# Kernel tuning notes

Measured on AMD Instinct MI355X. Metric: run time of the kernel, lower is better.

Reference implementation:

```python
import jax, jax.numpy as jnp
import numpy as np

NLON = 720  # output longitude points for irfft
B, C = 4, 8
LMAX, MMAX, NLAT = 360, 361, 361


def setup_inputs() -> dict:
    key = jax.random.key(0)
    kx, kd = jax.random.split(key)
    # x: real view of complex coeffs, shape [B, C, 2(vec comp), lmax, mmax, 2(re/im)]
    x = jax.random.normal(kx, (B, C, 2, LMAX, MMAX, 2), dtype=jnp.float32)
    # dpct: precomputed dLegendre buffer, shape [2, mmax, lmax, nlat]
    dpct = jax.random.normal(kd, (2, MMAX, LMAX, NLAT), dtype=jnp.float32) * 0.1
    return {"x": x, "dpct": dpct}


def reference(x, dpct):
    # split vector components and real/imag parts
    x0r = x[..., 0, :, :, 0]  # [..., lmax, mmax]
    x0i = x[..., 0, :, :, 1]
    x1r = x[..., 1, :, :, 0]
    x1i = x[..., 1, :, :, 1]
    d0 = dpct[0].astype(x.dtype)  # [mmax, lmax, nlat]
    d1 = dpct[1].astype(x.dtype)

    def ein(a, d):
        return jnp.einsum('...lm,mlk->...km', a, d)

    srl = ein(x0r, d0) - ein(x1i, d1)   # [..., nlat, mmax]
    sim = ein(x0i, d0) + ein(x1r, d1)
    trl = -ein(x0i, d1) - ein(x1r, d0)
    tim = ein(x0r, d1) - ein(x1i, d0)

    s = jax.lax.complex(srl, sim)
    t = jax.lax.complex(trl, tim)
    xs = jnp.stack((s, t), axis=-3)     # [..., 2, nlat, mmax] complex
    # inverse real FFT over longitude, 'forward' norm (no scaling on inverse)
    out = jnp.fft.irfft(xs, n=NLON, axis=-1, norm='forward')  # [..., 2, nlat, nlon]
    return out
```

## Files before the change

kernel.cpp:

```cpp
#include <hip/hip_runtime.h>
#include <hip/hip_bf16.h>
#include <math.h>

#define LMAX 360
#define MMAX 361
#define NLAT 361
#define NLON 720
#define BC   32
#define MT   (BC*2*NLAT)
#define NLATP 364
#define MTP  (BC*2*NLATP)
#define QT   722
#define KP   736
#define NP   768
#define BM   128
#define BN   128
#define BK   32

typedef __attribute__((ext_vector_type(8))) short short8;
typedef __attribute__((ext_vector_type(4))) short short4v;
typedef __attribute__((ext_vector_type(4))) float f32x4;

static __device__ __forceinline__ short f2bf(float v) {
    __hip_bfloat16 h = __float2bfloat16(v);
    return *reinterpret_cast<short*>(&h);
}

__global__ __launch_bounds__(256) void sht_prep_x(
    const float* __restrict__ x, __hip_bfloat16* __restrict__ xT)
{
    const int m0 = blockIdx.x * 32;
    const int l0 = blockIdx.y * 64;
    const int bc = blockIdx.z >> 1, f = blockIdx.z & 1;
    __shared__ float2 tile[64][33];
    const float2* __restrict__ x2 = (const float2*)x;
    const int t = threadIdx.x;
    const int rm = t & 31, rl = t >> 5;

    const int mm = min(m0 + rm, MMAX - 1);
    #pragma unroll
    for (int r = 0; r < 8; ++r) {
        int l = min(l0 + rl + r * 8, LMAX - 1);
        tile[rl + r * 8][rm] = x2[((size_t)(bc * 2 + f) * LMAX + l) * MMAX + mm];
    }
    __syncthreads();

    const int tm = t >> 3, lg = t & 7;
    const int m = m0 + tm;
    if (m >= MMAX) return;
    const int lw = l0 + lg * 8;
    if (lw >= LMAX) return;

    short8 re, im;
    #pragma unroll
    for (int e = 0; e < 8; ++e) {
        float2 v = tile[lg * 8 + e][tm];
        re[e] = f2bf(v.x);
        im[e] = f2bf(v.y);
    }
    size_t mb = (size_t)m * (128 * LMAX);
    *(short8*)((short*)xT + mb + (size_t)((f * 2 + 0) * 32 + bc) * LMAX + lw) = re;
    *(short8*)((short*)xT + mb + (size_t)((f * 2 + 1) * 32 + bc) * LMAX + lw) = im;
}

__global__ __launch_bounds__(256, 3) void sht_gemm1(
    const float* __restrict__ dpct, const __hip_bfloat16* __restrict__ xT,
    __hip_bfloat16* __restrict__ interQ)
{
    const int m  = blockIdx.x;
    const int K0 = blockIdx.y * 96;

    __shared__ __align__(16) char AlsB[96 * 128];
    __shared__ __align__(16) char BlsB[128 * 128];

    const int t    = threadIdx.x;
    const int lane = t & 63;
    const int wave = t >> 6;
    const int wm = (wave >> 1) * 48;
    const int wn = (wave & 1) * 64;
    const int fr = lane & 15;
    const int lq = lane >> 4;

    int kdv[3], lov[3], kcl[3];
    #pragma unroll
    for (int it = 0; it < 3; ++it) {
        int task = it * 256 + t;
        kdv[it] = task % 96;
        lov[it] = task / 96;
        kcl[it] = min(K0 + kdv[it], 360);
    }
    const int cB    = t >> 1;
    const int plane = cB >> 5, bcq = cB & 31;
    const int g0B   = (t & 1) * 4;

    const int            srcT[8] = {0, 1, 2, 3, 3, 2, 1, 0};
    const unsigned short sgnT[8] = {0, 0, 0x8000, 0x8000, 0x8000, 0, 0x8000, 0};

    f32x4 acc[3][4];
    const f32x4 zero = {0.f, 0.f, 0.f, 0.f};
    #pragma unroll
    for (int i = 0; i < 3; ++i)
        #pragma unroll
        for (int j = 0; j < 4; ++j) acc[i][j] = zero;

    float a0_[3][8], a1_[3][8];
    bool  v0_[3],    v1_[3];
    short8 bpf[4];
    bool   bvB[4];
    short  bsgn = 0;

#define STEP_P(s)  ((s) >= 6 ? 1 : 0)
#define STEP_L(s)  (((s) % 6) * 64)

#define LOAD_A(AP, LV, ss) {                                                   \
    const int p_ = STEP_P(ss); const int l0_ = STEP_L(ss);                     \
    const size_t rowb_ = ((size_t)p_ * MMAX + m) * LMAX;                       \
    _Pragma("unroll")                                                          \
    for (int it = 0; it < 3; ++it) {                                           \
        int lb_ = l0_ + lov[it] * 8;                                           \
        LV[it] = (lb_ < LMAX);                                                 \
        int lcl_ = LV[it] ? lb_ : 0;                                           \
        const float* sp_ = dpct + (rowb_ + lcl_) * (size_t)NLAT + kcl[it];     \
        _Pragma("unroll")                                                      \
        for (int e = 0; e < 8; ++e)                                            \
            AP[it][e] = sp_[(size_t)e * NLAT];                                 \
    } }

#define LOAD_B(ss) {                                                           \
    const int p_ = STEP_P(ss); const int l0_ = STEP_L(ss);                     \
    int src_ = srcT[p_ * 4 + plane];                                           \
    bsgn = (short)sgnT[p_ * 4 + plane];                                        \
    const short* bb_ = (const short*)xT + (size_t)m * (128 * LMAX) +           \
                       (size_t)(src_ * 32 + bcq) * LMAX;                       \
    _Pragma("unroll")                                                          \
    for (int i = 0; i < 4; ++i) {                                              \
        int lg2_ = l0_ + (g0B + i) * 8;                                        \
        bvB[i] = (lg2_ < LMAX);                                                \
        int lcl_ = bvB[i] ? lg2_ : 0;                                          \
        bpf[i] = *(const short8*)(bb_ + lcl_);                                 \
    } }

#define WRITE_A(AP, LV) {                                                      \
    _Pragma("unroll")                                                          \
    for (int it = 0; it < 3; ++it) {                                           \
        short8 w_;                                                             \
        _Pragma("unroll")                                                      \
        for (int e = 0; e < 8; ++e)                                            \
            w_[e] = LV[it] ? f2bf(AP[it][e]) : (short)0;                       \
        int kd_ = kdv[it], lo_ = lov[it];                                      \
        *(short8*)(AlsB + kd_ * 128 + ((lo_ ^ (kd_ & 7)) << 4)) = w_;          \
    } }

#define WRITE_B() {                                                            \
    _Pragma("unroll")                                                          \
    for (int i = 0; i < 4; ++i) {                                              \
        short8 v_ = bpf[i];                                                    \
        _Pragma("unroll")                                                      \
        for (int e = 0; e < 8; ++e) {                                          \
            short xe_ = (short)(v_[e] ^ bsgn);                                 \
            v_[e] = bvB[i] ? xe_ : (short)0;                                   \
        }                                                                      \
        int g_ = g0B + i;                                                      \
        *(short8*)(BlsB + cB * 128 + ((g_ ^ (cB & 7)) << 4)) = v_;             \
    } }

    auto compute = [&]() {
        #pragma unroll
        for (int kk = 0; kk < 2; ++kk) {
            short8 af[3], bg[4];
            const int g = kk * 4 + lq;
            #pragma unroll
            for (int mi = 0; mi < 3; ++mi) {
                int k = wm + mi * 16 + fr;
                af[mi] = *(const short8*)(AlsB + k * 128 + ((g ^ (k & 7)) << 4));
            }
            #pragma unroll
            for (int ni = 0; ni < 4; ++ni) {
                int c = wn + ni * 16 + fr;
                bg[ni] = *(const short8*)(BlsB + c * 128 + ((g ^ (c & 7)) << 4));
            }
            #pragma unroll
            for (int mi = 0; mi < 3; ++mi)
                #pragma unroll
                for (int ni = 0; ni < 4; ++ni)
                    acc[mi][ni] = __builtin_amdgcn_mfma_f32_16x16x32_bf16(
                        af[mi], bg[ni], acc[mi][ni], 0, 0, 0);
        }
    };

    LOAD_B(0);
    LOAD_A(a0_, v0_, 0);
    LOAD_A(a1_, v1_, 1);

    #pragma unroll 1
    for (int s = 0; s < 12; s += 2) {
        __syncthreads();
        WRITE_A(a0_, v0_);
        WRITE_B();
        __syncthreads();
        if (s + 1 < 12) LOAD_B(s + 1);
        if (s + 2 < 12) LOAD_A(a0_, v0_, s + 2);
        compute();

        __syncthreads();
        WRITE_A(a1_, v1_);
        WRITE_B();
        __syncthreads();
        if (s + 2 < 12) LOAD_B(s + 2);
        if (s + 3 < 12) LOAD_A(a1_, v1_, s + 3);
        compute();
    }

#undef LOAD_A
#undef LOAD_B
#undef WRITE_A
#undef WRITE_B
#undef STEP_P
#undef STEP_L

    #pragma unroll
    for (int mi = 0; mi < 3; ++mi) {
        int kr = K0 + wm + mi * 16 + lq * 4;
        #pragma unroll
        for (int ni = 0; ni < 4; ++ni) {
            int c = wn + ni * 16 + fr;
            int pl = c >> 5, bc = c & 31;
            int ri = pl & 1, tt = pl >> 1;
            size_t qb = (size_t)(2 * m + ri) * MTP + (size_t)(bc * 2 + tt) * NLATP;
            if (kr + 3 <= 360) {
                short4v w;
                #pragma unroll
                for (int r = 0; r < 4; ++r) w[r] = f2bf(acc[mi][ni][r]);
                *(short4v*)((short*)interQ + qb + kr) = w;
            } else if (kr <= 360) {
                ((short*)interQ)[qb + kr] = f2bf(acc[mi][ni][0]);
            }
        }
    }
}

__global__ __launch_bounds__(256) void sht_transpose(
    const __hip_bfloat16* __restrict__ inQ, __hip_bfloat16* __restrict__ outT)
{
    __shared__ __hip_bfloat16 tile[64][65];
    const int R0 = blockIdx.x * 64;
    const int q0 = blockIdx.y * 64;
    const int tx = threadIdx.x & 63;
    const int ty = threadIdx.x >> 6;
    const __hip_bfloat16 zv = __float2bfloat16(0.f);

    const int R  = R0 + tx;
    const int Rm = (R / NLAT) * NLATP + (R % NLAT);

    for (int qq = ty; qq < 64; qq += 4) {
        int q = q0 + qq;
        tile[qq][tx] = (q < QT) ? inQ[(size_t)q * MTP + Rm] : zv;
    }
    __syncthreads();
    if (q0 + tx < KP) {
        for (int rr = ty; rr < 64; rr += 4) {
            outT[(size_t)(R0 + rr) * KP + q0 + tx] = tile[tx][rr];
        }
    }
}

__global__ __launch_bounds__(256) void sht_make_w(__hip_bfloat16* __restrict__ W)
{
    const int idx = blockIdx.x * 256 + threadIdx.x;
    const int j = idx / KP;
    const int q = idx % KP;
    float v = 0.f;
    if (j < NLON && q < QT) {
        int m = q >> 1;
        float coef = (m == 0 || m == 360) ? 1.f : 2.f;
        int ph = (m * j) % 720;
        float ang = (float)ph * (float)(2.0 * M_PI / 720.0);
        float s, c;
        __sincosf(ang, &s, &c);
        v = (q & 1) ? (-coef * s) : (coef * c);
    }
    W[idx] = __float2bfloat16(v);
}

__global__ __launch_bounds__(256) void sht_gemm(
    const __hip_bfloat16* __restrict__ A,
    const __hip_bfloat16* __restrict__ W,
    float* __restrict__ out)
{
    __shared__ __align__(16) __hip_bfloat16 As[BM * BK];
    __shared__ __align__(16) __hip_bfloat16 Bs[BN * BK];
    const int t  = threadIdx.x;
    const int R0 = blockIdx.x * BM;
    const int J0 = blockIdx.y * BN;

    const int rowA = t >> 2;
    const int kc   = (t & 3) * 8;
    const int gr0  = min(R0 + rowA,      MT - 1);
    const int gr1  = min(R0 + rowA + 64, MT - 1);
    const __hip_bfloat16* pa0 = A + (size_t)gr0 * KP + kc;
    const __hip_bfloat16* pa1 = A + (size_t)gr1 * KP + kc;
    const __hip_bfloat16* pb0 = W + (size_t)(J0 + rowA) * KP + kc;
    const __hip_bfloat16* pb1 = W + (size_t)(J0 + rowA + 64) * KP + kc;

    const int lane = t & 63;
    const int wave = t >> 6;
    const int wm = (wave >> 1) * 64;
    const int wn = (wave & 1) * 64;
    const int fr = lane & 15;
    const int kg = (lane >> 4) * 8;

    f32x4 acc[4][4];
    const f32x4 zero = {0.f, 0.f, 0.f, 0.f};
    #pragma unroll
    for (int i = 0; i < 4; ++i)
        #pragma unroll
        for (int j = 0; j < 4; ++j) acc[i][j] = zero;

    short8 va0 = *(const short8*)pa0;
    short8 va1 = *(const short8*)pa1;
    short8 vb0 = *(const short8*)pb0;
    short8 vb1 = *(const short8*)pb1;

    for (int kt = 0; kt < KP / BK; ++kt) {
        __syncthreads();
        *(short8*)&As[t * 8]        = va0;
        *(short8*)&As[t * 8 + 2048] = va1;
        *(short8*)&Bs[t * 8]        = vb0;
        *(short8*)&Bs[t * 8 + 2048] = vb1;
        __syncthreads();

        if (kt + 1 < KP / BK) {
            const int ko = (kt + 1) * BK;
            va0 = *(const short8*)(pa0 + ko);
            va1 = *(const short8*)(pa1 + ko);
            vb0 = *(const short8*)(pb0 + ko);
            vb1 = *(const short8*)(pb1 + ko);
        }

        short8 af[4], bg[4];
        #pragma unroll
        for (int i = 0; i < 4; ++i)
            af[i] = *(const short8*)&As[(wm + i * 16 + fr) * BK + kg];
        #pragma unroll
        for (int i = 0; i < 4; ++i)
            bg[i] = *(const short8*)&Bs[(wn + i * 16 + fr) * BK + kg];

        #pragma unroll
        for (int mi = 0; mi < 4; ++mi)
            #pragma unroll
            for (int ni = 0; ni < 4; ++ni)
                acc[mi][ni] = __builtin_amdgcn_mfma_f32_16x16x32_bf16(
                    af[mi], bg[ni], acc[mi][ni], 0, 0, 0);
    }

    const int orow = (lane >> 4) * 4;
    #pragma unroll
    for (int mi = 0; mi < 4; ++mi) {
        #pragma unroll
        for (int ni = 0; ni < 4; ++ni) {
            #pragma unroll
            for (int r = 0; r < 4; ++r) {
                int row = R0 + wm + mi * 16 + orow + r;
                int col = J0 + wn + ni * 16 + fr;
                if (row < MT && col < NLON)
                    out[(size_t)row * NLON + col] = acc[mi][ni][r];
            }
        }
    }
}

extern "C" void kernel_launch(void* const* d_in, const int* in_sizes, int n_in,
                              void* d_out, int out_size, void* d_ws, size_t ws_size,
                              hipStream_t stream)
{
    const float* x    = (const float*)d_in[0];
    const float* dpct = (const float*)d_in[1];
    float* out        = (float*)d_out;

    char* ws = (char*)d_ws;
    __hip_bfloat16* xT     = (__hip_bfloat16*)ws;
    __hip_bfloat16* interT = (__hip_bfloat16*)(ws + 34009088);
    __hip_bfloat16* interQ = (__hip_bfloat16*)(ws + 70254592);
    __hip_bfloat16* Wt     = (__hip_bfloat16*)(ws + 104857600);

    dim3 gp(12, 6, 64);
    sht_prep_x<<<gp, 256, 0, stream>>>(x, xT);

    dim3 g1(MMAX, 4);
    sht_gemm1<<<g1, 256, 0, stream>>>(dpct, xT, interQ);

    dim3 gt(MT / 64, 12);
    sht_transpose<<<gt, 256, 0, stream>>>(interQ, interT);

    sht_make_w<<<(NP * KP) / 256, 256, 0, stream>>>(Wt);

    dim3 gg((MT + BM - 1) / BM, NP / BN);
    sht_gemm<<<gg, 256, 0, stream>>>(interT, Wt, out);
}
```

Before: 322.0 us.

## Load both Legendre planes per step and reuse each x tile across them

Each pipeline step of the first GEMM now loads both dpct planes into two shared-memory A tiles and loads the x tile once. The source-plane permutation and sign flip are applied when B fragments are read during compute, instead of when B is staged. This halves the number of steps and barriers and removes the second global load of the same x tile. In exchange it uses more shared memory and registers, which may lower occupancy under the 3-blocks launch bound, and adds XOR work to the inner loop.

```diff
diff --git a/kernel.cpp b/kernel.cpp
--- a/kernel.cpp
+++ b/kernel.cpp
@@ -70,7 +70,8 @@
     const int m  = blockIdx.x;
     const int K0 = blockIdx.y * 96;
 
-    __shared__ __align__(16) char AlsB[96 * 128];
+    __shared__ __align__(16) char Als0[96 * 128];
+    __shared__ __align__(16) char Als1[96 * 128];
     __shared__ __align__(16) char BlsB[128 * 128];
 
     const int t    = threadIdx.x;
@@ -89,9 +90,8 @@
         lov[it] = task / 96;
         kcl[it] = min(K0 + kdv[it], 360);
     }
-    const int cB    = t >> 1;
-    const int plane = cB >> 5, bcq = cB & 31;
-    const int g0B   = (t & 1) * 4;
+    const int cB  = t >> 1;
+    const int g0B = (t & 1) * 4;
 
     const int            srcT[8] = {0, 1, 2, 3, 3, 2, 1, 0};
     const unsigned short sgnT[8] = {0, 0, 0x8000, 0x8000, 0x8000, 0, 0x8000, 0};
@@ -103,63 +103,56 @@
         #pragma unroll
         for (int j = 0; j < 4; ++j) acc[i][j] = zero;
 
-    float a0_[3][8], a1_[3][8];
-    bool  v0_[3],    v1_[3];
+    float  a0_[3][8], a1_[3][8];
+    bool   av_[3];
     short8 bpf[4];
     bool   bvB[4];
-    short  bsgn = 0;
-
-#define STEP_P(s)  ((s) >= 6 ? 1 : 0)
-#define STEP_L(s)  (((s) % 6) * 64)
-
-#define LOAD_A(AP, LV, ss) {                                                   \
-    const int p_ = STEP_P(ss); const int l0_ = STEP_L(ss);                     \
-    const size_t rowb_ = ((size_t)p_ * MMAX + m) * LMAX;                       \
-    _Pragma("unroll")                                                          \
-    for (int it = 0; it < 3; ++it) {                                           \
-        int lb_ = l0_ + lov[it] * 8;                                           \
-        LV[it] = (lb_ < LMAX);                                                 \
-        int lcl_ = LV[it] ? lb_ : 0;                                           \
-        const float* sp_ = dpct + (rowb_ + lcl_) * (size_t)NLAT + kcl[it];     \
-        _Pragma("unroll")                                                      \
-        for (int e = 0; e < 8; ++e)                                            \
-            AP[it][e] = sp_[(size_t)e * NLAT];                                 \
-    } }
-
-#define LOAD_B(ss) {                                                           \
-    const int p_ = STEP_P(ss); const int l0_ = STEP_L(ss);                     \
-    int src_ = srcT[p_ * 4 + plane];                                           \
-    bsgn = (short)sgnT[p_ * 4 + plane];                                        \
+
+#define LOAD_AB(ss) {                                                          \
+    const int l0_ = (ss) * 64;                                                 \
     const short* bb_ = (const short*)xT + (size_t)m * (128 * LMAX) +           \
-                       (size_t)(src_ * 32 + bcq) * LMAX;                       \
+                       (size_t)cB * LMAX;                                      \
     _Pragma("unroll")                                                          \
     for (int i = 0; i < 4; ++i) {                                              \
         int lg2_ = l0_ + (g0B + i) * 8;                                        \
         bvB[i] = (lg2_ < LMAX);                                                \
         int lcl_ = bvB[i] ? lg2_ : 0;                                          \
         bpf[i] = *(const short8*)(bb_ + lcl_);                                 \
-    } }
-
-#define WRITE_A(AP, LV) {                                                      \
+    }                                                                          \
     _Pragma("unroll")                                                          \
     for (int it = 0; it < 3; ++it) {                                           \
-        short8 w_;                                                             \
+        int lb_ = l0_ + lov[it] * 8;                                           \
+        av_[it] = (lb_ < LMAX);                                                \
+        int lcl_ = av_[it] ? lb_ : 0;                                          \
+        const float* s0_ = dpct + ((size_t)m * LMAX + lcl_) * NLAT + kcl[it];  \
+        const float* s1_ = dpct + (((size_t)MMAX + m) * LMAX + lcl_) * NLAT    \
+                           + kcl[it];                                          \
         _Pragma("unroll")                                                      \
-        for (int e = 0; e < 8; ++e)                                            \
-            w_[e] = LV[it] ? f2bf(AP[it][e]) : (short)0;                       \
+        for (int e = 0; e < 8; ++e) {                                          \
+            a0_[it][e] = s0_[(size_t)e * NLAT];                                \
+            a1_[it][e] = s1_[(size_t)e * NLAT];                                \
+        }                                                                      \
+    } }
+
+#define WRITE_AB() {                                                           \
+    _Pragma("unroll")                                                          \
+    for (int it = 0; it < 3; ++it) {                                           \
+        short8 w0_, w1_;                                                       \
+        _Pragma("unroll")                                                      \
+        for (int e = 0; e < 8; ++e) {                                          \
+            w0_[e] = av_[it] ? f2bf(a0_[it][e]) : (short)0;                    \
+            w1_[e] = av_[it] ? f2bf(a1_[it][e]) : (short)0;                    \
+        }                                                                      \
         int kd_ = kdv[it], lo_ = lov[it];                                      \
-        *(short8*)(AlsB + kd_ * 128 + ((lo_ ^ (kd_ & 7)) << 4)) = w_;          \
-    } }
-
-#define WRITE_B() {                                                            \
+        int off_ = kd_ * 128 + ((lo_ ^ (kd_ & 7)) << 4);                       \
+        *(short8*)(Als0 + off_) = w0_;                                         \
+        *(short8*)(Als1 + off_) = w1_;                                         \
+    }                                                                          \
     _Pragma("unroll")                                                          \
     for (int i = 0; i < 4; ++i) {                                              \
         short8 v_ = bpf[i];                                                    \
         _Pragma("unroll")                                                      \
-        for (int e = 0; e < 8; ++e) {                                          \
-            short xe_ = (short)(v_[e] ^ bsgn);                                 \
-            v_[e] = bvB[i] ? xe_ : (short)0;                                   \
-        }                                                                      \
+        for (int e = 0; e < 8; ++e) v_[e] = bvB[i] ? v_[e] : (short)0;         \
         int g_ = g0B + i;                                                      \
         *(short8*)(BlsB + cB * 128 + ((g_ ^ (cB & 7)) << 4)) = v_;             \
     } }
@@ -167,56 +160,48 @@
     auto compute = [&]() {
         #pragma unroll
         for (int kk = 0; kk < 2; ++kk) {
-            short8 af[3], bg[4];
             const int g = kk * 4 + lq;
+            short8 af0[3], af1[3];
             #pragma unroll
             for (int mi = 0; mi < 3; ++mi) {
                 int k = wm + mi * 16 + fr;
-                af[mi] = *(const short8*)(AlsB + k * 128 + ((g ^ (k & 7)) << 4));
+                int off = k * 128 + ((g ^ (k & 7)) << 4);
+                af0[mi] = *(const short8*)(Als0 + off);
+                af1[mi] = *(const short8*)(Als1 + off);
             }
             #pragma unroll
-            for (int ni = 0; ni < 4; ++ni) {
-                int c = wn + ni * 16 + fr;
-                bg[ni] = *(const short8*)(BlsB + c * 128 + ((g ^ (c & 7)) << 4));
+            for (int h = 0; h < 2; ++h) {
+                #pragma unroll
+                for (int ni = 0; ni < 4; ++ni) {
+                    int pl = 2 * (wave & 1) + (ni >> 1);
+                    int rB = srcT[h * 4 + pl] * 32 + (ni & 1) * 16 + fr;
+                    short8 bg = *(const short8*)(
+                        BlsB + rB * 128 + ((g ^ (rB & 7)) << 4));
+                    short sg = (short)sgnT[h * 4 + pl];
+                    #pragma unroll
+                    for (int e = 0; e < 8; ++e) bg[e] ^= sg;
+                    #pragma unroll
+                    for (int mi = 0; mi < 3; ++mi)
+                        acc[mi][ni] = __builtin_amdgcn_mfma_f32_16x16x32_bf16(
+                            h ? af1[mi] : af0[mi], bg, acc[mi][ni], 0, 0, 0);
+                }
             }
-            #pragma unroll
-            for (int mi = 0; mi < 3; ++mi)
-                #pragma unroll
-                for (int ni = 0; ni < 4; ++ni)
-                    acc[mi][ni] = __builtin_amdgcn_mfma_f32_16x16x32_bf16(
-                        af[mi], bg[ni], acc[mi][ni], 0, 0, 0);
         }
     };
 
-    LOAD_B(0);
-    LOAD_A(a0_, v0_, 0);
-    LOAD_A(a1_, v1_, 1);
+    LOAD_AB(0);
 
     #pragma unroll 1
-    for (int s = 0; s < 12; s += 2) {
+    for (int s = 0; s < 6; ++s) {
         __syncthreads();
-        WRITE_A(a0_, v0_);
-        WRITE_B();
+        WRITE_AB();
         __syncthreads();
-        if (s + 1 < 12) LOAD_B(s + 1);
-        if (s + 2 < 12) LOAD_A(a0_, v0_, s + 2);
+        if (s < 5) LOAD_AB(s + 1);
         compute();
-
-        __syncthreads();
-        WRITE_A(a1_, v1_);
-        WRITE_B();
-        __syncthreads();
-        if (s + 2 < 12) LOAD_B(s + 2);
-        if (s + 3 < 12) LOAD_A(a1_, v1_, s + 3);
-        compute();
-    }
-
-#undef LOAD_A
-#undef LOAD_B
-#undef WRITE_A
-#undef WRITE_B
-#undef STEP_P
-#undef STEP_L
+    }
+
+#undef LOAD_AB
+#undef WRITE_AB
 
     #pragma unroll
     for (int mi = 0; mi < 3; ++mi) {
```

New measurement: 397.4 us. 23.4% more time.
